# Kernel optimization log

Hardware: AMD Instinct MI355X
Metric: run time of the kernel (lower is better)

Reference implementation:

```python
import jax, jax.numpy as jnp
import numpy as np

NEG = -1e30
H = 768

def mask_logits(target, mask):
    return target * mask + (1.0 - mask) * NEG

def setup_inputs() -> dict:
    key = jax.random.key(0)
    ks = jax.random.split(key, 8)
    B, CL, QL = 16, 512, 64
    c = jax.random.normal(ks[0], (B, CL, H), dtype=jnp.float32)
    q = jax.random.normal(ks[1], (B, QL, H), dtype=jnp.float32)
    c_mask = jnp.ones((B, CL), dtype=jnp.float32)
    q_mask = jnp.ones((B, QL), dtype=jnp.float32)
    # nn.Linear(768,1) weights (kaiming-ish scale) and biases
    std = 1.0 / np.sqrt(H)
    w_c = jax.random.normal(ks[2], (H,), dtype=jnp.float32) * std
    w_q = jax.random.normal(ks[3], (H,), dtype=jnp.float32) * std
    w_cq = jax.random.normal(ks[4], (H,), dtype=jnp.float32) * std
    b_c = jax.random.normal(ks[5], (), dtype=jnp.float32) * std
    b_q = jax.random.normal(ks[6], (), dtype=jnp.float32) * std
    b_cq = jax.random.normal(ks[7], (), dtype=jnp.float32) * std
    return {"c": c, "q": q, "c_mask": c_mask, "q_mask": q_mask,
            "w_c": w_c, "b_c": b_c, "w_q": w_q, "b_q": b_q,
            "w_cq": w_cq, "b_cq": b_cq}

def reference(c, q, c_mask, q_mask, w_c, b_c, w_q, b_q, w_cq, b_cq):
    # c: (B, c_len, H), q: (B, q_len, H)
    cm = c_mask[:, :, None]   # (B, c_len, 1)
    qm = q_mask[:, None, :]   # (B, 1, q_len)
    # per-query loop in torch == trilinear term: ((c*w_cq) @ q^T) + b_cq
    cq = jnp.einsum('bid,bjd->bij', c * w_cq, q) + b_cq      # (B, c_len, q_len)
    s = (c @ w_c + b_c)[:, :, None] + (q @ w_q + b_q)[:, None, :] + cq
    a = jax.nn.softmax(mask_logits(s, qm), axis=2)            # (B, c_len, q_len)
    c2q = jnp.einsum('bij,bjd->bid', a, q)                    # (B, c_len, H)
    b_att = jax.nn.softmax(jnp.max(mask_logits(s, cm), axis=2), axis=1)  # (B, c_len)
    q2c = jnp.einsum('bi,bid->bd', b_att, c)[:, None, :]      # (B, 1, H)
    x = jnp.concatenate([c, c2q, c * c2q, c * q2c], axis=-1)  # (B, c_len, 4H)
    return x
```

## Files before the change

kernel.cpp:

```cpp
#include <hip/hip_runtime.h>
#include <math.h>
#include <stdint.h>

#define NEGV -1e30f
typedef unsigned short u16;
typedef unsigned int u32;
typedef short bfx8 __attribute__((ext_vector_type(8)));
typedef float f32x4 __attribute__((ext_vector_type(4)));

constexpr int B_  = 16;
constexpr int CL  = 512;
constexpr int QL  = 64;
constexpr int H   = 768;
constexpr int OD  = 4 * H;
constexpr int IT  = 16;
constexpr int OSTR = 772;

constexpr size_t WS_QW     = 0;
constexpr size_t WS_ROWMAX = 1024;
constexpr size_t WS_PART   = 17408;
constexpr size_t WS_Q2C    = 410624;
constexpr size_t WS_QBF    = 422912;
constexpr size_t WS_QTF    = 816128;

__device__ __forceinline__ u16 f2b(float x) {
  u32 u = __float_as_uint(x);
  u += 0x7FFFu + ((u >> 16) & 1u);
  return (u16)(u >> 16);
}
__device__ __forceinline__ float wredmax(float v) {
#pragma unroll
  for (int off = 32; off; off >>= 1) v = fmaxf(v, __shfl_xor(v, off));
  return v;
}
__device__ __forceinline__ float wredsum(float v) {
#pragma unroll
  for (int off = 32; off; off >>= 1) v += __shfl_xor(v, off);
  return v;
}

__global__ __launch_bounds__(256) void k_qprep(const float* __restrict__ q,
                                               const float* __restrict__ w_cq,
                                               const float* __restrict__ w_q,
                                               const float* __restrict__ b_q,
                                               const float* __restrict__ b_cq,
                                               u16* __restrict__ qbF,
                                               u16* __restrict__ qTF,
                                               float* __restrict__ qw) {
  const int ch = blockIdx.x, bb = blockIdx.y, t = threadIdx.x;
  if (ch == 6) {
    int j = t >> 2, qt = t & 3;
    const float* qr = q + ((size_t)bb * QL + j) * H;
    float s = 0.f;
#pragma unroll 8
    for (int p = 0; p < 48; ++p) {
      float4 v = *(const float4*)(qr + (qt * 48 + p) * 4);
      float4 w = *(const float4*)(w_q + (qt * 48 + p) * 4);
      s += v.x * w.x + v.y * w.y + v.z * w.z + v.w * w.w;
    }
    s += __shfl_xor(s, 1);
    s += __shfl_xor(s, 2);
    if (qt == 0) qw[bb * QL + j] = s + b_q[0] + b_cq[0];
    return;
  }
  __shared__ u16 tR[64 * 132], tS[64 * 132];
  const int d0 = ch * 128;
#pragma unroll
  for (int s2 = 0; s2 < 8; ++s2) {
    int idx = t + s2 * 256, j = idx >> 5, d4 = idx & 31;
    size_t go = ((size_t)(bb * QL + j)) * H + d0 + d4 * 4;
    float4 v = *(const float4*)(q + go);
    float4 w = *(const float4*)(w_cq + d0 + d4 * 4);
    uint2 raw, scl;
    raw.x = f2b(v.x) | ((u32)f2b(v.y) << 16);
    raw.y = f2b(v.z) | ((u32)f2b(v.w) << 16);
    scl.x = f2b(v.x * w.x) | ((u32)f2b(v.y * w.y) << 16);
    scl.y = f2b(v.z * w.z) | ((u32)f2b(v.w * w.w) << 16);
    *(uint2*)&tR[j * 132 + d4 * 4] = raw;
    *(uint2*)&tS[j * 132 + d4 * 4] = scl;
  }
  __syncthreads();
  {
    int l = t & 63, jt = t >> 6, lr = l & 15, lg = l >> 4;
#pragma unroll
    for (int kt = 0; kt < 4; ++kt) {
      u16 vals[8];
#pragma unroll
      for (int e = 0; e < 8; ++e)
        vals[e] = tS[(jt * 16 + lr) * 132 + kt * 32 + lg * 8 + e];
      uint4 pk;
      pk.x = vals[0] | ((u32)vals[1] << 16);
      pk.y = vals[2] | ((u32)vals[3] << 16);
      pk.z = vals[4] | ((u32)vals[5] << 16);
      pk.w = vals[6] | ((u32)vals[7] << 16);
      *(uint4*)(qbF + ((((size_t)bb * 4 + jt) * 24) + ch * 4 + kt) * 512 + l * 8) = pk;
    }
  }
  {
#pragma unroll
    for (int rep = 0; rep < 4; ++rep) {
      int idx = rep * 256 + t;
      int l = idx & 63, h = (idx >> 6) & 1, uul = idx >> 7;
      int lr = l & 15, lg = l >> 4;
      u16 vals[8];
#pragma unroll
      for (int e = 0; e < 8; ++e)
        vals[e] = tR[(h * 32 + lg * 8 + e) * 132 + uul * 16 + lr];
      uint4 pk;
      pk.x = vals[0] | ((u32)vals[1] << 16);
      pk.y = vals[2] | ((u32)vals[3] << 16);
      pk.z = vals[4] | ((u32)vals[5] << 16);
      pk.w = vals[6] | ((u32)vals[7] << 16);
      *(uint4*)(qTF + (((size_t)bb * 48 + ch * 8 + uul) * 2 + h) * 512 + l * 8) = pk;
    }
  }
}

__global__ __launch_bounds__(256, 2) void ka(const float* __restrict__ c,
                                             const float* __restrict__ c_mask,
                                             const float* __restrict__ q_mask,
                                             const float* __restrict__ w_c,
                                             const float* __restrict__ b_c,
                                             const float* __restrict__ qw,
                                             const u16* __restrict__ qbF,
                                             const u16* __restrict__ qTF,
                                             float* __restrict__ rowmax,
                                             float* __restrict__ out) {
  __shared__ __align__(16) char shm[8 * OSTR * 4];
  __shared__ float sS[IT * 68];
  __shared__ u16 aS[IT * 64];
  float* oS = (float*)shm;

  const int t = threadIdx.x, lane = t & 63;
  const int wid = __builtin_amdgcn_readfirstlane(t >> 6);
  const int bb = blockIdx.y, i0 = blockIdx.x * IT;
  const int lr = lane & 15, lg = lane >> 4;
  const int sw = (lr & 7) << 4;

  float cwq = 0.f;
  {
    int row = t >> 4, c4b = t & 15;
    size_t cb0 = ((size_t)bb * CL + i0 + row) * H;
#pragma unroll
    for (int u = 0; u < 12; ++u) {
      int col4 = c4b + u * 16;
      float4 v = *(const float4*)(c + cb0 + col4 * 4);
      float4 w = *(const float4*)(w_c + col4 * 4);
      cwq += v.x * w.x + v.y * w.y + v.z * w.z + v.w * w.w;
      uint2 pk;
      pk.x = f2b(v.x) | ((u32)f2b(v.y) << 16);
      pk.y = f2b(v.z) | ((u32)f2b(v.w) << 16);
      int byte = row * 1536 + ((col4 * 8) ^ ((row & 7) << 4));
      *(uint2*)(shm + byte) = pk;
    }
    cwq += __shfl_xor(cwq, 1);
    cwq += __shfl_xor(cwq, 2);
    cwq += __shfl_xor(cwq, 4);
    cwq += __shfl_xor(cwq, 8);
  }
  const float qw_r = qw[bb * QL + lane];
  const float qm_r = q_mask[bb * QL + lane];
  const float bc = b_c[0];
  __syncthreads();

  f32x4 acc0 = {0.f, 0.f, 0.f, 0.f}, acc1 = {0.f, 0.f, 0.f, 0.f};
  {
    const u16* qbp = qbF + (((size_t)bb * 4 + wid) * 24) * 512 + lane * 8;
    const char* ap = shm + lr * 1536;
#pragma unroll
    for (int kt = 0; kt < 24; kt += 2) {
      bfx8 av0 = *(const bfx8*)(ap + ((kt * 64 + lg * 16) ^ sw));
      bfx8 av1 = *(const bfx8*)(ap + (((kt + 1) * 64 + lg * 16) ^ sw));
      bfx8 bv0 = *(const bfx8*)(qbp + kt * 512);
      bfx8 bv1 = *(const bfx8*)(qbp + (kt + 1) * 512);
      acc0 = __builtin_amdgcn_mfma_f32_16x16x32_bf16(av0, bv0, acc0, 0, 0, 0);
      acc1 = __builtin_amdgcn_mfma_f32_16x16x32_bf16(av1, bv1, acc1, 0, 0, 0);
    }
  }
#pragma unroll
  for (int m = 0; m < 4; ++m)
    sS[(lg * 4 + m) * 68 + wid * 16 + lr] = acc0[m] + acc1[m];
  __syncthreads();

#pragma unroll
  for (int rr = 0; rr < 4; ++rr) {
    int r = wid * 4 + rr;
    float s = sS[r * 68 + lane] + qw_r;
    float mraw = wredmax(s);
    float sm = (qm_r > 0.5f) ? s : NEGV;
    float mm = wredmax(sm);
    float p = __expf(sm - mm);
    float ps = wredsum(p);
    float a = p / ps;
    float cwr = __shfl(cwq, rr * 16);
    if (lane == 0) {
      float cmv = c_mask[bb * CL + i0 + r];
      rowmax[bb * CL + i0 + r] = (cmv > 0.5f) ? (mraw + cwr + bc) : NEGV;
    }
    int byte = r * 128 + ((lane * 2) ^ ((r & 7) << 4));
    *(u16*)((char*)aS + byte) = f2b(a);
  }
  __syncthreads();

  bfx8 a0 = *(const bfx8*)((char*)aS + lr * 128 + ((lg * 16) ^ sw));
  bfx8 a1 = *(const bfx8*)((char*)aS + lr * 128 + ((64 + lg * 16) ^ sw));
  const u16* qtp = qTF + (size_t)bb * 49152 + lane * 8;
  f32x4 o[12];
#pragma unroll
  for (int u = 0; u < 12; ++u) {
    int uu = wid * 12 + u;
    bfx8 b0 = *(const bfx8*)(qtp + (size_t)uu * 1024);
    bfx8 b1 = *(const bfx8*)(qtp + (size_t)uu * 1024 + 512);
    f32x4 v = {0.f, 0.f, 0.f, 0.f};
    v = __builtin_amdgcn_mfma_f32_16x16x32_bf16(a0, b0, v, 0, 0, 0);
    v = __builtin_amdgcn_mfma_f32_16x16x32_bf16(a1, b1, v, 0, 0, 0);
    o[u] = v;
  }

#pragma unroll
  for (int p = 0; p < 2; ++p) {
    if (p) __syncthreads();
#pragma unroll
    for (int u = 0; u < 12; ++u) {
      int d = wid * 192 + u * 16 + lr;
      oS[(lg * 2 + 0) * OSTR + d] = o[u][2 * p];
      oS[(lg * 2 + 1) * OSTR + d] = o[u][2 * p + 1];
    }
    __syncthreads();
    int row8 = t >> 5, c32 = t & 31;
    int g = row8 >> 1, mo = row8 & 1;
    int ri = g * 4 + 2 * p + mo;
    size_t grow = (size_t)bb * CL + i0 + ri;
    const float* crow = c + grow * H;
    float* ob = out + grow * OD;
#pragma unroll
    for (int k = 0; k < 6; ++k) {
      int d = (c32 + k * 32) * 4;
      float4 cv = *(const float4*)(crow + d);
      float4 ov = *(const float4*)&oS[row8 * OSTR + d];
      *(float4*)(ob + d) = cv;
      *(float4*)(ob + H + d) = ov;
      *(float4*)(ob + 2 * H + d) = make_float4(cv.x * ov.x, cv.y * ov.y,
                                               cv.z * ov.z, cv.w * ov.w);
    }
  }
}

__global__ __launch_bounds__(256) void kb(const float* __restrict__ rowmax,
                                          const float* __restrict__ c,
                                          float* __restrict__ part) {
  int s = blockIdx.x, b = blockIdx.y, t = threadIdx.x;
  __shared__ float red[8];
  __shared__ float ba[16];
  float v0 = rowmax[b * CL + t], v1 = rowmax[b * CL + t + 256];
  float m = wredmax(fmaxf(v0, v1));
  if ((t & 63) == 0) red[t >> 6] = m;
  __syncthreads();
  m = fmaxf(fmaxf(red[0], red[1]), fmaxf(red[2], red[3]));
  float p = __expf(v0 - m) + __expf(v1 - m);
  p = wredsum(p);
  if ((t & 63) == 0) red[4 + (t >> 6)] = p;
  __syncthreads();
  float ssum = red[4] + red[5] + red[6] + red[7];
  if (t < 16) ba[t] = __expf(rowmax[b * CL + s * 16 + t] - m) / ssum;
  __syncthreads();
  if (t < 192) {
    const float* cb = c + ((size_t)b * CL + s * 16) * H;
    float4 acc = make_float4(0.f, 0.f, 0.f, 0.f);
#pragma unroll
    for (int r = 0; r < 16; ++r) {
      float w = ba[r];
      float4 cv = *(const float4*)(cb + (size_t)r * H + t * 4);
      acc.x += w * cv.x; acc.y += w * cv.y; acc.z += w * cv.z; acc.w += w * cv.w;
    }
    *(float4*)(part + ((size_t)b * 32 + s) * H + t * 4) = acc;
  }
}

__global__ __launch_bounds__(256) void kb3(const float* __restrict__ part,
                                           float* __restrict__ q2c) {
  int b = blockIdx.x / 3, third = blockIdx.x % 3, t = threadIdx.x;
  int d = third * 256 + t;
  float s = 0.f;
  for (int k = 0; k < 32; ++k) s += part[((size_t)b * 32 + k) * H + d];
  q2c[b * H + d] = s;
}

__global__ __launch_bounds__(256) void kc(const float* __restrict__ c,
                                          const float* __restrict__ q2c,
                                          float* __restrict__ out) {
  const float4* c4 = (const float4*)c;
  const float4* g4 = (const float4*)q2c;
  float4* o4 = (float4*)out;
  int idx = blockIdx.x * 256 + threadIdx.x;
#pragma unroll
  for (int k = 0; k < 3; ++k, idx += 2048 * 256) {
    int row = idx / 192, dq = idx - row * 192;
    int b = row >> 9;
    float4 cv = c4[(size_t)row * 192 + dq];
    float4 gv = g4[b * 192 + dq];
    float4 r;
    r.x = cv.x * gv.x; r.y = cv.y * gv.y; r.z = cv.z * gv.z; r.w = cv.w * gv.w;
    o4[(size_t)row * 768 + 576 + dq] = r;
  }
}

extern "C" void kernel_launch(void* const* d_in, const int* in_sizes, int n_in,
                              void* d_out, int out_size, void* d_ws, size_t ws_size,
                              hipStream_t stream) {
  const float* c      = (const float*)d_in[0];
  const float* q      = (const float*)d_in[1];
  const float* c_mask = (const float*)d_in[2];
  const float* q_mask = (const float*)d_in[3];
  const float* w_c    = (const float*)d_in[4];
  const float* b_c    = (const float*)d_in[5];
  const float* w_q    = (const float*)d_in[6];
  const float* b_q    = (const float*)d_in[7];
  const float* w_cq   = (const float*)d_in[8];
  const float* b_cq   = (const float*)d_in[9];
  float* out = (float*)d_out;
  float* ws  = (float*)d_ws;
  float* qw     = ws + WS_QW;
  float* rowmax = ws + WS_ROWMAX;
  float* part   = ws + WS_PART;
  float* q2c    = ws + WS_Q2C;
  u16*   qbF    = (u16*)(ws + WS_QBF);
  u16*   qTF    = (u16*)(ws + WS_QTF);

  k_qprep<<<dim3(7, B_), 256, 0, stream>>>(q, w_cq, w_q, b_q, b_cq, qbF, qTF, qw);
  ka<<<dim3(CL / IT, B_), 256, 0, stream>>>(c, c_mask, q_mask, w_c, b_c,
                                            qw, qbF, qTF, rowmax, out);
  kb<<<dim3(32, B_), 256, 0, stream>>>(rowmax, c, part);
  kb3<<<B_ * 3, 256, 0, stream>>>(part, q2c);
  kc<<<2048, 256, 0, stream>>>(c, q2c, out);
}
```

Measured before the change: 61.13 us.

## Fuse q2c reduction into final output kernel and prefetch B fragments in ka

Merges the kb3 partial-sum reduction and the kc elementwise kernel into a single kc2 kernel. Each block reduces its 128-column slice of the partial sums into shared memory, then writes c*q2c for 32 rows, which removes one launch and the q2c workspace round trip. In ka, the first q-fragment loads for both MFMA phases are issued early to hide global latency. The two-pass output staging is replaced by one pass, which doubles the shared buffer size and may lower occupancy. kc2 also recomputes the same reduction redundantly in each of the 16 row-group blocks.

```diff
diff --git a/kernel.cpp b/kernel.cpp
--- a/kernel.cpp
+++ b/kernel.cpp
@@ -19,7 +19,6 @@
 constexpr size_t WS_QW     = 0;
 constexpr size_t WS_ROWMAX = 1024;
 constexpr size_t WS_PART   = 17408;
-constexpr size_t WS_Q2C    = 410624;
 constexpr size_t WS_QBF    = 422912;
 constexpr size_t WS_QTF    = 816128;
 
@@ -126,7 +125,7 @@
                                              const u16* __restrict__ qTF,
                                              float* __restrict__ rowmax,
                                              float* __restrict__ out) {
-  __shared__ __align__(16) char shm[8 * OSTR * 4];
+  __shared__ __align__(16) char shm[IT * OSTR * 4];
   __shared__ float sS[IT * 68];
   __shared__ u16 aS[IT * 64];
   float* oS = (float*)shm;
@@ -136,6 +135,12 @@
   const int bb = blockIdx.y, i0 = blockIdx.x * IT;
   const int lr = lane & 15, lg = lane >> 4;
   const int sw = (lr & 7) << 4;
+
+  const u16* qbp = qbF + (((size_t)bb * 4 + wid) * 24) * 512 + lane * 8;
+  const u16* qtp = qTF + (size_t)bb * 49152 + lane * 8;
+
+  bfx8 qpf0 = *(const bfx8*)(qbp);
+  bfx8 qpf1 = *(const bfx8*)(qbp + 512);
 
   float cwq = 0.f;
   {
@@ -165,10 +170,13 @@
 
   f32x4 acc0 = {0.f, 0.f, 0.f, 0.f}, acc1 = {0.f, 0.f, 0.f, 0.f};
   {
-    const u16* qbp = qbF + (((size_t)bb * 4 + wid) * 24) * 512 + lane * 8;
     const char* ap = shm + lr * 1536;
-#pragma unroll
-    for (int kt = 0; kt < 24; kt += 2) {
+    acc0 = __builtin_amdgcn_mfma_f32_16x16x32_bf16(
+        *(const bfx8*)(ap + ((lg * 16) ^ sw)), qpf0, acc0, 0, 0, 0);
+    acc1 = __builtin_amdgcn_mfma_f32_16x16x32_bf16(
+        *(const bfx8*)(ap + ((64 + lg * 16) ^ sw)), qpf1, acc1, 0, 0, 0);
+#pragma unroll
+    for (int kt = 2; kt < 24; kt += 2) {
       bfx8 av0 = *(const bfx8*)(ap + ((kt * 64 + lg * 16) ^ sw));
       bfx8 av1 = *(const bfx8*)(ap + (((kt + 1) * 64 + lg * 16) ^ sw));
       bfx8 bv0 = *(const bfx8*)(qbp + kt * 512);
@@ -177,6 +185,10 @@
       acc1 = __builtin_amdgcn_mfma_f32_16x16x32_bf16(av1, bv1, acc1, 0, 0, 0);
     }
   }
+  bfx8 pf0 = *(const bfx8*)(qtp + (size_t)(wid * 12 + 0) * 1024);
+  bfx8 pf1 = *(const bfx8*)(qtp + (size_t)(wid * 12 + 0) * 1024 + 512);
+  bfx8 pf2 = *(const bfx8*)(qtp + (size_t)(wid * 12 + 1) * 1024);
+  bfx8 pf3 = *(const bfx8*)(qtp + (size_t)(wid * 12 + 1) * 1024 + 512);
 #pragma unroll
   for (int m = 0; m < 4; ++m)
     sS[(lg * 4 + m) * 68 + wid * 16 + lr] = acc0[m] + acc1[m];
@@ -204,10 +216,19 @@
 
   bfx8 a0 = *(const bfx8*)((char*)aS + lr * 128 + ((lg * 16) ^ sw));
   bfx8 a1 = *(const bfx8*)((char*)aS + lr * 128 + ((64 + lg * 16) ^ sw));
-  const u16* qtp = qTF + (size_t)bb * 49152 + lane * 8;
   f32x4 o[12];
-#pragma unroll
-  for (int u = 0; u < 12; ++u) {
+  {
+    f32x4 v0 = {0.f, 0.f, 0.f, 0.f};
+    v0 = __builtin_amdgcn_mfma_f32_16x16x32_bf16(a0, pf0, v0, 0, 0, 0);
+    v0 = __builtin_amdgcn_mfma_f32_16x16x32_bf16(a1, pf1, v0, 0, 0, 0);
+    o[0] = v0;
+    f32x4 v1 = {0.f, 0.f, 0.f, 0.f};
+    v1 = __builtin_amdgcn_mfma_f32_16x16x32_bf16(a0, pf2, v1, 0, 0, 0);
+    v1 = __builtin_amdgcn_mfma_f32_16x16x32_bf16(a1, pf3, v1, 0, 0, 0);
+    o[1] = v1;
+  }
+#pragma unroll
+  for (int u = 2; u < 12; ++u) {
     int uu = wid * 12 + u;
     bfx8 b0 = *(const bfx8*)(qtp + (size_t)uu * 1024);
     bfx8 b1 = *(const bfx8*)(qtp + (size_t)uu * 1024 + 512);
@@ -218,26 +239,23 @@
   }
 
 #pragma unroll
-  for (int p = 0; p < 2; ++p) {
-    if (p) __syncthreads();
-#pragma unroll
-    for (int u = 0; u < 12; ++u) {
-      int d = wid * 192 + u * 16 + lr;
-      oS[(lg * 2 + 0) * OSTR + d] = o[u][2 * p];
-      oS[(lg * 2 + 1) * OSTR + d] = o[u][2 * p + 1];
-    }
-    __syncthreads();
-    int row8 = t >> 5, c32 = t & 31;
-    int g = row8 >> 1, mo = row8 & 1;
-    int ri = g * 4 + 2 * p + mo;
-    size_t grow = (size_t)bb * CL + i0 + ri;
+  for (int u = 0; u < 12; ++u) {
+    int d = wid * 192 + u * 16 + lr;
+#pragma unroll
+    for (int m = 0; m < 4; ++m)
+      oS[(lg * 4 + m) * OSTR + d] = o[u][m];
+  }
+  __syncthreads();
+  {
+    int row = t >> 4, c4b = t & 15;
+    size_t grow = (size_t)bb * CL + i0 + row;
     const float* crow = c + grow * H;
     float* ob = out + grow * OD;
 #pragma unroll
-    for (int k = 0; k < 6; ++k) {
-      int d = (c32 + k * 32) * 4;
+    for (int k = 0; k < 12; ++k) {
+      int d = (c4b + k * 16) * 4;
       float4 cv = *(const float4*)(crow + d);
-      float4 ov = *(const float4*)&oS[row8 * OSTR + d];
+      float4 ov = *(const float4*)&oS[row * OSTR + d];
       *(float4*)(ob + d) = cv;
       *(float4*)(ob + H + d) = ov;
       *(float4*)(ob + 2 * H + d) = make_float4(cv.x * ov.x, cv.y * ov.y,
@@ -277,31 +295,43 @@
   }
 }
 
-__global__ __launch_bounds__(256) void kb3(const float* __restrict__ part,
-                                           float* __restrict__ q2c) {
-  int b = blockIdx.x / 3, third = blockIdx.x % 3, t = threadIdx.x;
-  int d = third * 256 + t;
-  float s = 0.f;
-  for (int k = 0; k < 32; ++k) s += part[((size_t)b * 32 + k) * H + d];
-  q2c[b * H + d] = s;
-}
-
-__global__ __launch_bounds__(256) void kc(const float* __restrict__ c,
-                                          const float* __restrict__ q2c,
-                                          float* __restrict__ out) {
-  const float4* c4 = (const float4*)c;
-  const float4* g4 = (const float4*)q2c;
-  float4* o4 = (float4*)out;
-  int idx = blockIdx.x * 256 + threadIdx.x;
-#pragma unroll
-  for (int k = 0; k < 3; ++k, idx += 2048 * 256) {
-    int row = idx / 192, dq = idx - row * 192;
-    int b = row >> 9;
-    float4 cv = c4[(size_t)row * 192 + dq];
-    float4 gv = g4[b * 192 + dq];
-    float4 r;
-    r.x = cv.x * gv.x; r.y = cv.y * gv.y; r.z = cv.z * gv.z; r.w = cv.w * gv.w;
-    o4[(size_t)row * 768 + 576 + dq] = r;
+__global__ __launch_bounds__(256) void kc2(const float* __restrict__ part,
+                                           const float* __restrict__ c,
+                                           float* __restrict__ out) {
+  __shared__ float4 redS[8][32];
+  __shared__ float4 q2cS[32];
+  const int b = blockIdx.y;
+  const int s = blockIdx.x >> 4, rg = blockIdx.x & 15;
+  const int t = threadIdx.x;
+  const int grp = t >> 5, col4 = t & 31;
+  float4 acc = make_float4(0.f, 0.f, 0.f, 0.f);
+#pragma unroll
+  for (int u = 0; u < 4; ++u) {
+    float4 v = *(const float4*)(part + ((size_t)b * 32 + grp * 4 + u) * H +
+                                s * 128 + col4 * 4);
+    acc.x += v.x; acc.y += v.y; acc.z += v.z; acc.w += v.w;
+  }
+  redS[grp][col4] = acc;
+  __syncthreads();
+  if (t < 32) {
+    float4 sum = redS[0][t];
+#pragma unroll
+    for (int g = 1; g < 8; ++g) {
+      float4 v = redS[g][t];
+      sum.x += v.x; sum.y += v.y; sum.z += v.z; sum.w += v.w;
+    }
+    q2cS[t] = sum;
+  }
+  __syncthreads();
+  float4 gv = q2cS[col4];
+  const int sub = t >> 5;
+#pragma unroll
+  for (int r2 = 0; r2 < 4; ++r2) {
+    int row = rg * 32 + sub * 4 + r2;
+    size_t grow = (size_t)b * CL + row;
+    float4 cv = *(const float4*)(c + grow * H + s * 128 + col4 * 4);
+    *(float4*)(out + grow * OD + 3 * H + s * 128 + col4 * 4) =
+        make_float4(cv.x * gv.x, cv.y * gv.y, cv.z * gv.z, cv.w * gv.w);
   }
 }
 
@@ -323,7 +353,6 @@
   float* qw     = ws + WS_QW;
   float* rowmax = ws + WS_ROWMAX;
   float* part   = ws + WS_PART;
-  float* q2c    = ws + WS_Q2C;
   u16*   qbF    = (u16*)(ws + WS_QBF);
   u16*   qTF    = (u16*)(ws + WS_QTF);
 
@@ -331,6 +360,5 @@
   ka<<<dim3(CL / IT, B_), 256, 0, stream>>>(c, c_mask, q_mask, w_c, b_c,
                                             qw, qbF, qTF, rowmax, out);
   kb<<<dim3(32, B_), 256, 0, stream>>>(rowmax, c, part);
-  kb3<<<B_ * 3, 256, 0, stream>>>(part, q2c);
-  kc<<<2048, 256, 0, stream>>>(c, q2c, out);
-}
+  kc2<<<dim3(96, B_), 256, 0, stream>>>(part, c, out);
+}
```

Result: faster. 58.26 us (-4.7%).
